# Kernel optimization log

Hardware: AMD Instinct MI355X
Metric: run time of the kernel (lower is better)

Reference implementation:

```python
import jax, jax.numpy as jnp
import numpy as np

DIM = 256
HEADS = 8
HEAD_DIM = DIM // HEADS
WS = 7            # window size
SHIFT = 3         # shift size
H = 56
W = 56
B = 32
WA = WS * WS      # window area = 49
NWH, NWW = H // WS, W // WS
NW = NWH * NWW    # windows per image


def _make_attn_mask():
    # replicate the torch mask construction for the shifted windows
    img = np.zeros((H, W), dtype=np.float32)
    cnt = 0
    for hs in (slice(0, -WS), slice(-WS, -SHIFT), slice(-SHIFT, None)):
        for ws_ in (slice(0, -WS), slice(-WS, -SHIFT), slice(-SHIFT, None)):
            img[hs, ws_] = cnt
            cnt += 1
    mw = img.reshape(NWH, WS, NWW, WS).transpose(0, 2, 1, 3).reshape(-1, WA)  # (nW, 49)
    diff = mw[:, None, :] - mw[:, :, None]                                    # (nW, 49, 49)
    return np.where(diff != 0, -100.0, 0.0).astype(np.float32)


def _make_rel_index():
    coords = np.stack(np.meshgrid(np.arange(WS), np.arange(WS), indexing='ij')).reshape(2, -1)
    rel = coords[:, :, None] - coords[:, None, :]        # (2, 49, 49)
    rel = rel.transpose(1, 2, 0) + (WS - 1)              # shift to >= 0
    rel[..., 0] *= 2 * WS - 1
    return rel.sum(-1).astype(np.int32)                  # (49, 49) in [0, 169)


def setup_inputs() -> dict:
    key = jax.random.key(0)
    ks = jax.random.split(key, 12)
    s = 0.02
    inp = {
        'x': jax.random.normal(ks[0], (B, H, W, DIM), dtype=jnp.float32),
        'ln1_w': jnp.ones((DIM,), jnp.float32), 'ln1_b': jnp.zeros((DIM,), jnp.float32),
        'qkv_w': s * jax.random.normal(ks[1], (3 * DIM, DIM), jnp.float32),
        'qkv_b': jnp.zeros((3 * DIM,), jnp.float32),
        'rpb_table': s * jax.random.normal(ks[2], ((2 * WS - 1) ** 2, HEADS), jnp.float32),
        'proj_w': s * jax.random.normal(ks[3], (DIM, DIM), jnp.float32),
        'proj_b': jnp.zeros((DIM,), jnp.float32),
        'ln2_w': jnp.ones((DIM,), jnp.float32), 'ln2_b': jnp.zeros((DIM,), jnp.float32),
        'fc1_w': s * jax.random.normal(ks[4], (4 * DIM, DIM), jnp.float32),
        'fc1_b': jnp.zeros((4 * DIM,), jnp.float32),
        'ln3_w': jnp.ones((4 * DIM,), jnp.float32), 'ln3_b': jnp.zeros((4 * DIM,), jnp.float32),
        'fc2_w': s * jax.random.normal(ks[5], (DIM, 4 * DIM), jnp.float32),
        'fc2_b': jnp.zeros((DIM,), jnp.float32),
        'attn_mask': jnp.asarray(_make_attn_mask()),     # (nW, 49, 49)
        'rel_index': jnp.asarray(_make_rel_index()),     # (49, 49) int32
    }
    return inp


def _ln(x, w, b, eps=1e-5):
    m = jnp.mean(x, axis=-1, keepdims=True)
    v = jnp.mean((x - m) ** 2, axis=-1, keepdims=True)
    return (x - m) * jax.lax.rsqrt(v + eps) * w + b


def reference(x, ln1_w, ln1_b, qkv_w, qkv_b, rpb_table, proj_w, proj_b,
              ln2_w, ln2_b, fc1_w, fc1_b, ln3_w, ln3_b, fc2_w, fc2_b,
              attn_mask, rel_index):
    Bn, Hn, Wn, C = x.shape
    # ---- attention branch ----
    y = _ln(x, ln1_w, ln1_b)
    sh = jnp.roll(y, (-SHIFT, -SHIFT), axis=(1, 2))
    # window partition: (B, H, W, C) -> (B*nW, 49, C)
    win = sh.reshape(Bn, NWH, WS, NWW, WS, C).transpose(0, 1, 3, 2, 4, 5).reshape(Bn * NW, WA, C)
    qkv = win @ qkv_w.T + qkv_b                              # (Bw, 49, 3C)
    qkv = qkv.reshape(Bn * NW, WA, 3, HEADS, HEAD_DIM).transpose(2, 0, 3, 1, 4)
    q, k, v = qkv[0], qkv[1], qkv[2]                         # (Bw, h, 49, d)
    scale = HEAD_DIM ** -0.5
    attn = jnp.einsum('bhqd,bhkd->bhqk', q * scale, k)       # (Bw, h, 49, 49)
    bias = rpb_table[rel_index]                              # (49, 49, h)
    attn = attn + jnp.transpose(bias, (2, 0, 1))[None]
    attn = attn.reshape(Bn, NW, HEADS, WA, WA) + attn_mask[None, :, None]
    attn = jax.nn.softmax(attn, axis=-1).reshape(Bn * NW, HEADS, WA, WA)
    out = jnp.einsum('bhqk,bhkd->bhqd', attn, v)             # (Bw, h, 49, d)
    out = out.transpose(0, 2, 1, 3).reshape(Bn * NW, WA, C)
    out = out @ proj_w.T + proj_b
    # window reverse + un-shift
    out = out.reshape(Bn, NWH, NWW, WS, WS, C).transpose(0, 1, 3, 2, 4, 5).reshape(Bn, Hn, Wn, C)
    out = jnp.roll(out, (SHIFT, SHIFT), axis=(1, 2))
    x = x + out
    # ---- MLP branch (note: extra LayerNorm inside MLP per source) ----
    z = _ln(x, ln2_w, ln2_b)
    h = jax.nn.gelu(z @ fc1_w.T + fc1_b, approximate=False)
    h = _ln(h, ln3_w, ln3_b)
    x = x + (h @ fc2_w.T + fc2_b)
    return x
```

## Files before the change

kernel.cpp:

```cpp
#include <hip/hip_runtime.h>
#include <hip/hip_bf16.h>
#include <math.h>

typedef __attribute__((ext_vector_type(8))) short bf16x8;
typedef __attribute__((ext_vector_type(4))) float f32x4;
typedef __attribute__((ext_vector_type(4))) float f4;
typedef __attribute__((ext_vector_type(8))) unsigned short us8;
typedef __attribute__((ext_vector_type(4))) unsigned short us4;
typedef unsigned short u16;
typedef unsigned int u32;

#define HEADS 8
#define SHIFT_ 3
#define HIMG 56
#define WIMG 56
#define WA 49
#define NTOK 100352
#define NPAIR 16384

static __device__ __forceinline__ float bf2f(u16 v){ return __uint_as_float(((u32)v)<<16); }
static __device__ __forceinline__ u16 f2bf(float f){
  u32 u = __float_as_uint(f);
  return (u16)((u + 0x7fffu + ((u>>16)&1u)) >> 16);
}
static __device__ __forceinline__ float wsum(float v){
  #pragma unroll
  for (int off=32; off>0; off>>=1) v += __shfl_xor(v, off, 64);
  return v;
}
static __device__ __forceinline__ void glds16(const u16* g, u16* l){
  __builtin_amdgcn_global_load_lds(
      (const __attribute__((address_space(1))) unsigned int*)g,
      (__attribute__((address_space(3))) unsigned int*)l, 16, 0, 0);
}
static __device__ __forceinline__ int tok2pix(int row){
  int bw = row / 49, t = row - bw*49;
  int b  = bw >> 6,  w = bw & 63;
  int wh = w >> 3,   ww = w & 7;
  int th = t / 7,    tw = t - th*7;
  int r = wh*7 + th + SHIFT_; if (r >= HIMG) r -= HIMG;
  int c = ww*7 + tw + SHIFT_; if (c >= WIMG) c -= WIMG;
  return (b*HIMG + r)*WIMG + c;
}
static __device__ __forceinline__ float gelu_f(float x){
  float x2 = x*x;
  float u  = x*(0.7978845608028654f + 0.0356774081363001f*x2);
  float e  = __expf(u+u);
  float th = 1.0f - 2.0f*__builtin_amdgcn_rcpf(1.0f+e);
  return 0.5f*x*(1.0f+th);
}

template<int C, int ISBF>
__global__ void ln_stats_kernel(const void* __restrict__ srcv, float* __restrict__ stats){
  int wave = threadIdx.x >> 6, lane = threadIdx.x & 63;
  int tok = blockIdx.x*4 + wave;
  float s=0.f, s2=0.f;
  if (ISBF == 0){
    const float* p = (const float*)srcv + (size_t)tok*C;
    #pragma unroll
    for (int i=0;i<C/256;i++){
      f4 v = *(const f4*)(p + lane*4*(C/256) + i*4);
      #pragma unroll
      for (int e=0;e<4;e++){ float f=v[e]; s+=f; s2+=f*f; }
    }
  } else {
    const u16* p = (const u16*)srcv + (size_t)tok*C;
    #pragma unroll
    for (int i=0;i<C/512;i++){
      us8 v = *(const us8*)(p + lane*8*(C/512) + i*8);
      #pragma unroll
      for (int e=0;e<8;e++){ float f=bf2f(v[e]); s+=f; s2+=f*f; }
    }
  }
  s = wsum(s); s2 = wsum(s2);
  if (lane==0){
    float mean = s/(float)C;
    float var  = s2/(float)C - mean*mean;
    stats[2*tok]   = mean;
    stats[2*tok+1] = rsqrtf(var + 1e-5f);
  }
}

__global__ void ln_apply_kernel(const float* __restrict__ src, u16* __restrict__ dst){
  int wave = threadIdx.x >> 6, lane = threadIdx.x & 63;
  int tok = blockIdx.x*4 + wave;
  const float* p = src + (size_t)tok*256;
  f4 a = *(const f4*)(p + lane*4);
  float s = a[0]+a[1]+a[2]+a[3];
  float s2 = a[0]*a[0]+a[1]*a[1]+a[2]*a[2]+a[3]*a[3];
  s = wsum(s); s2 = wsum(s2);
  float mean = s*(1.f/256.f);
  float var  = s2*(1.f/256.f) - mean*mean;
  float rstd = rsqrtf(var + 1e-5f);
  us4 o;
  #pragma unroll
  for (int e=0;e<4;e++) o[e] = f2bf((a[e]-mean)*rstd);
  *(us4*)(dst + (size_t)tok*256 + lane*4) = o;
}

__global__ void prep_weights(
    const float* __restrict__ qkv_w, const float* __restrict__ qkv_b,
    const float* __restrict__ ln1w,  const float* __restrict__ ln1b,
    const float* __restrict__ fc1_w, const float* __restrict__ fc1_b,
    const float* __restrict__ ln2w,  const float* __restrict__ ln2b,
    const float* __restrict__ fc2_w, const float* __restrict__ fc2_b,
    const float* __restrict__ ln3w,  const float* __restrict__ ln3b,
    const float* __restrict__ proj_w, const float* __restrict__ proj_b,
    u16* __restrict__ wq, float* __restrict__ bq,
    u16* __restrict__ w1, float* __restrict__ b1,
    u16* __restrict__ w2, float* __restrict__ b2,
    u16* __restrict__ wp, float* __restrict__ bp,
    float* __restrict__ cs2)
{
  int wave = threadIdx.x>>6, lane = threadIdx.x&63;
  int n = blockIdx.x*4 + wave;
  const float *W,*lw,*lb,*bs; u16* WO; float* BO; int K, row, noln, docs;
  if (n < 768)      { W=qkv_w; lw=ln1w; lb=ln1b; bs=qkv_b; WO=wq; BO=bq; K=256;  row=n;      noln=0; docs=0; }
  else if (n < 1792){ W=fc1_w; lw=ln2w; lb=ln2b; bs=fc1_b; WO=w1; BO=b1; K=256;  row=n-768;  noln=0; docs=0; }
  else if (n < 2048){ W=fc2_w; lw=ln3w; lb=ln3b; bs=fc2_b; WO=w2; BO=b2; K=1024; row=n-1792; noln=0; docs=1; }
  else              { W=proj_w; lw=nullptr; lb=nullptr; bs=proj_b; WO=wp; BO=bp; K=256; row=n-2048; noln=1; docs=0; }
  float dot = 0.f, cs = 0.f;
  for (int k=lane; k<K; k+=64){
    float wv = W[(size_t)row*K + k];
    if (noln){
      WO[(size_t)row*K + k] = f2bf(wv);
    } else {
      dot += wv * lb[k];
      u16 q = f2bf(wv * lw[k]);
      WO[(size_t)row*K + k] = q;
      cs += bf2f(q);
    }
  }
  dot = wsum(dot);
  if (docs){ cs = wsum(cs); if (lane==0) cs2[row] = cs; }
  if (lane==0) BO[row] = bs[row] + dot;
}

template<int SMODE, int EPI>
__global__ __launch_bounds__(256)
void gemm6(const void* __restrict__ Av, const u16* __restrict__ Bt,
           const float* __restrict__ stats, const float* __restrict__ biasf,
           const float* __restrict__ resid, const float* __restrict__ colsum,
           void* __restrict__ outv, int K, int NT, int CHUNK)
{
  constexpr int BM=128, BN=128, BK=64;
  __shared__ u16 smem[16384];
  u16* As = smem;
  u16* Bs = smem + 8192;
  int b = blockIdx.x;
  int linear = (b & 7)*CHUNK + (b >> 3);
  int mt = linear / NT, nt = linear - mt*NT;
  int m0 = mt*BM, n0 = nt*BN;
  int tid  = threadIdx.x;
  int lane = tid & 63, wave = tid >> 6;
  int wr = wave >> 1, wc = wave & 1;
  int lc16 = lane & 15, g = lane >> 4;
  int nsteps = K >> 6;

  const u16* asrc[4];
  const u16* bsrc[4];
  #pragma unroll
  for (int i=0;i<4;i++){
    int c = tid + i*256;
    int row = c >> 3, ch = (c & 7) ^ (row & 7);
    if (SMODE <= 1){
      int grow = (SMODE==0) ? tok2pix(m0+row) : (m0+row);
      asrc[i] = (const u16*)Av + (size_t)grow*K + ch*8;
    }
    bsrc[i] = Bt + (size_t)(n0+row)*K + ch*8;
  }
  float smean[4], srstd[4];
  if (SMODE == 3){
    #pragma unroll
    for (int i=0;i<4;i++){
      int grow = m0 + ((tid + i*256) >> 3);
      smean[i] = stats[2*grow]; srstd[i] = stats[2*grow+1];
    }
  }

  f32x4 acc[4][4];
  #pragma unroll
  for (int i=0;i<4;i++)
    #pragma unroll
    for (int j=0;j<4;j++){ acc[i][j][0]=0.f; acc[i][j][1]=0.f; acc[i][j][2]=0.f; acc[i][j][3]=0.f; }

  f4 rcurf[4][2];
  if (SMODE == 3){
    #pragma unroll
    for (int i=0;i<4;i++){
      int c = tid + i*256; int row = c>>3, ch = c&7;
      const float* ap = (const float*)Av + (size_t)(m0+row)*K + ch*8;
      rcurf[i][0] = *(const f4*)ap; rcurf[i][1] = *(const f4*)(ap+4);
    }
  }

  for (int t=0; t<nsteps; ++t){
    int kt = t << 6;
    if (SMODE <= 1){
      #pragma unroll
      for (int i=0;i<4;i++) glds16(asrc[i]+kt, As + i*2048 + wave*512);
    } else {
      #pragma unroll
      for (int i=0;i<4;i++){
        int c = tid + i*256; int row = c>>3, ch = c&7;
        us8 o;
        #pragma unroll
        for (int e=0;e<8;e++){
          float fv = rcurf[i][e>>2][e&3];
          o[e] = f2bf((fv - smean[i])*srstd[i]);
        }
        u32 byte = (u32)(row*128 + ch*16) ^ ((u32)(row&7)<<4);
        *(us8*)(As + (byte>>1)) = o;
      }
    }
    #pragma unroll
    for (int i=0;i<4;i++) glds16(bsrc[i]+kt, Bs + i*2048 + wave*512);
    __syncthreads();
    if (SMODE == 3 && t+1 < nsteps){
      int kt1 = kt + 64;
      f4 rnextf[4][2];
      #pragma unroll
      for (int i=0;i<4;i++){
        int c = tid + i*256; int row = c>>3, ch = c&7;
        const float* ap = (const float*)Av + (size_t)(m0+row)*K + kt1 + ch*8;
        rnextf[i][0] = *(const f4*)ap; rnextf[i][1] = *(const f4*)(ap+4);
      }
      #pragma unroll
      for (int kk=0; kk<2; kk++){
        bf16x8 af[4], bfr[4];
        #pragma unroll
        for (int mi=0;mi<4;mi++){
          int r = wr*64 + mi*16 + lc16;
          u32 byte = (u32)(r*128 + kk*64 + g*16) ^ ((u32)(r&7)<<4);
          af[mi] = *(const bf16x8*)(As + (byte>>1));
        }
        #pragma unroll
        for (int ni=0;ni<4;ni++){
          int r = wc*64 + ni*16 + lc16;
          u32 byte = (u32)(r*128 + kk*64 + g*16) ^ ((u32)(r&7)<<4);
          bfr[ni] = *(const bf16x8*)(Bs + (byte>>1));
        }
        #pragma unroll
        for (int mi=0;mi<4;mi++)
          #pragma unroll
          for (int ni=0;ni<4;ni++)
            acc[mi][ni] = __builtin_amdgcn_mfma_f32_16x16x32_bf16(af[mi], bfr[ni], acc[mi][ni], 0, 0, 0);
      }
      #pragma unroll
      for (int i=0;i<4;i++){ rcurf[i][0] = rnextf[i][0]; rcurf[i][1] = rnextf[i][1]; }
    } else {
      #pragma unroll
      for (int kk=0; kk<2; kk++){
        bf16x8 af[4], bfr[4];
        #pragma unroll
        for (int mi=0;mi<4;mi++){
          int r = wr*64 + mi*16 + lc16;
          u32 byte = (u32)(r*128 + kk*64 + g*16) ^ ((u32)(r&7)<<4);
          af[mi] = *(const bf16x8*)(As + (byte>>1));
        }
        #pragma unroll
        for (int ni=0;ni<4;ni++){
          int r = wc*64 + ni*16 + lc16;
          u32 byte = (u32)(r*128 + kk*64 + g*16) ^ ((u32)(r&7)<<4);
          bfr[ni] = *(const bf16x8*)(Bs + (byte>>1));
        }
        #pragma unroll
        for (int mi=0;mi<4;mi++)
          #pragma unroll
          for (int ni=0;ni<4;ni++)
            acc[mi][ni] = __builtin_amdgcn_mfma_f32_16x16x32_bf16(af[mi], bfr[ni], acc[mi][ni], 0, 0, 0);
      }
    }
    __syncthreads();
  }

  int lr = lane >> 4;
  if (EPI==0 || EPI==2){
    u16* Cs = smem;
    #pragma unroll
    for (int mi=0;mi<4;mi++){
      #pragma unroll
      for (int ni=0;ni<4;ni++){
        int cl = wc*64 + ni*16 + lc16;
        float bv = biasf[n0 + cl];
        #pragma unroll
        for (int j=0;j<4;j++){
          int rl = wr*64 + mi*16 + lr*4 + j;
          float v = acc[mi][ni][j] + bv;
          if (EPI==2) v = gelu_f(v);
          u32 byte = (u32)(rl*256 + cl*2) ^ ((u32)(rl&7)<<4);
          Cs[byte>>1] = f2bf(v);
        }
      }
    }
    __syncthreads();
    #pragma unroll
    for (int i=0;i<8;i++){
      int c = tid + i*256;
      int rl = c>>4, c0 = (c&15)*8;
      u32 byte = (u32)(rl*256 + c0*2) ^ ((u32)(rl&7)<<4);
      us8 v = *(const us8*)(Cs + (byte>>1));
      int row = m0 + rl, col = n0 + c0;
      if (EPI==0){
        int which = col>>8, hh = (col>>5)&7, d0 = col&31;
        int bwi = row/49, t = row - bwi*49;
        *(us8*)((u16*)outv + ((size_t)which*NPAIR + bwi*8 + hh)*(WA*32) + t*32 + d0) = v;
      } else {
        *(us8*)((u16*)outv + (size_t)row*1024 + col) = v;
      }
    }
  } else {
    float* Cs = (float*)smem;
    #pragma unroll
    for (int hp=0; hp<2; hp++){
      if (hp) __syncthreads();
      if (wc == hp){
        float bv4[4], cs4[4];
        #pragma unroll
        for (int ni=0;ni<4;ni++){
          int col = n0 + hp*64 + ni*16 + lc16;
          bv4[ni] = biasf[col];
          if (EPI==4) cs4[ni] = colsum[col];
        }
        #pragma unroll
        for (int mi=0;mi<4;mi++){
          #pragma unroll
          for (int j=0;j<4;j++){
            int rl = wr*64 + mi*16 + lr*4 + j;
            float rs = 1.f, mmrs = 0.f;
            if (EPI==4){
              int grow = m0 + rl;
              rs = stats[2*grow+1];
              mmrs = stats[2*grow]*rs;
            }
            #pragma unroll
            for (int ni=0;ni<4;ni++){
              int cl = ni*16 + lc16;
              float v;
              if (EPI==4) v = acc[mi][ni][j]*rs + bv4[ni] - mmrs*cs4[ni];
              else        v = acc[mi][ni][j] + bv4[ni];
              u32 byte = (u32)(rl*256 + cl*4) ^ ((u32)(rl&7)<<4);
              *(float*)((char*)Cs + byte) = v;
            }
          }
        }
      }
      __syncthreads();
      #pragma unroll
      for (int i=0;i<8;i++){
        int c = tid + i*256;
        int row = c>>4, ch = c&15;
        u32 byte = (u32)(row*256 + ch*16) ^ ((u32)(row&7)<<4);
        f4 v = *(const f4*)((const char*)Cs + byte);
        int grow = m0 + row, col = n0 + hp*64 + ch*4;
        size_t addr;
        if (EPI==1) addr = (size_t)tok2pix(grow)*256 + col;
        else        addr = (size_t)grow*256 + col;
        f4 rr = *(const f4*)(resid + addr);
        v += rr;
        *(f4*)((float*)outv + addr) = v;
      }
    }
  }
}

__global__ void attn_mfma_kernel(
    const u16* __restrict__ qkv,
    const float* __restrict__ rpb,
    const int* __restrict__ rel,
    const float* __restrict__ mask,
    u16* __restrict__ outb)
{
  __shared__ u16 Kls[4][64*32];
  __shared__ u16 Vt [4][32*64];
  __shared__ u16 Pls[4][64*64];
  int wave = threadIdx.x>>6, lane = threadIdx.x&63;
  int pair = blockIdx.x*4 + wave;
  int bw = pair>>3, h = pair&7, w = bw&63;
  int lc = lane&15, g = lane>>4;
  const u16* qg = qkv + (size_t)pair*(WA*32);
  const u16* kg = qg + (size_t)NPAIR*(WA*32);
  const u16* vg = qg + (size_t)2*NPAIR*(WA*32);
  u16* Kp = &Kls[wave][0];
  u16* Vp = &Vt[wave][0];
  u16* Pp = &Pls[wave][0];

  #pragma unroll
  for (int i=0;i<4;i++){
    int idx = i*64 + lane;
    int r = idx>>2, seg = idx&3;
    us8 kv, vv;
    if (r < WA){
      kv = *(const us8*)(kg + r*32 + seg*8);
      vv = *(const us8*)(vg + r*32 + seg*8);
    } else {
      #pragma unroll
      for (int e=0;e<8;e++){ kv[e]=0; vv[e]=0; }
    }
    *(us8*)(Kp + r*32 + seg*8) = kv;
    #pragma unroll
    for (int e=0;e<8;e++){
      int d = seg*8 + e;
      u32 byte = ((u32)(d*128 + r*2)) ^ ((u32)(d&7)<<4);
      Vp[byte>>1] = vv[e];
    }
  }

  bf16x8 qa[4];
  #pragma unroll
  for (int mi=0;mi<4;mi++){
    int r = mi*16 + lc;
    if (r < WA) qa[mi] = *(const bf16x8*)(qg + r*32 + g*8);
    else { bf16x8 z;
           #pragma unroll
           for (int e=0;e<8;e++) z[e]=0; qa[mi]=z; }
  }

  f32x4 acc[4][4];
  #pragma unroll
  for (int i=0;i<4;i++)
    #pragma unroll
    for (int j=0;j<4;j++){ acc[i][j][0]=0.f; acc[i][j][1]=0.f; acc[i][j][2]=0.f; acc[i][j][3]=0.f; }
  __syncthreads();
  #pragma unroll
  for (int ni=0;ni<4;ni++){
    bf16x8 kb = *(const bf16x8*)(Kp + (ni*16+lc)*32 + g*8);
    #pragma unroll
    for (int mi=0;mi<4;mi++)
      acc[mi][ni] = __builtin_amdgcn_mfma_f32_16x16x32_bf16(qa[mi], kb, acc[mi][ni], 0, 0, 0);
  }

  const float scale = 0.17677669529663689f;
  float rinv[4][4];
  #pragma unroll
  for (int mi=0;mi<4;mi++){
    #pragma unroll
    for (int jr=0;jr<4;jr++){
      int i = mi*16 + g*4 + jr;
      float sv[4];
      #pragma unroll
      for (int ni=0;ni<4;ni++){
        int j = ni*16 + lc;
        float s;
        if (i < WA && j < WA){
          s = acc[mi][ni][jr]*scale + rpb[rel[i*WA+j]*8 + h] + mask[((size_t)w*WA + i)*WA + j];
        } else s = -1e9f;
        sv[ni] = s;
      }
      float mx = fmaxf(fmaxf(sv[0],sv[1]), fmaxf(sv[2],sv[3]));
      #pragma unroll
      for (int off=1; off<16; off<<=1) mx = fmaxf(mx, __shfl_xor(mx, off, 64));
      float sum = 0.f;
      #pragma unroll
      for (int ni=0;ni<4;ni++){ sv[ni] = __expf(sv[ni]-mx); sum += sv[ni]; }
      #pragma unroll
      for (int off=1; off<16; off<<=1) sum += __shfl_xor(sum, off, 64);
      rinv[mi][jr] = __builtin_amdgcn_rcpf(sum);
      #pragma unroll
      for (int ni=0;ni<4;ni++){
        int j = ni*16 + lc;
        u32 byte = ((u32)(i*128 + j*2)) ^ ((u32)(i&7)<<4);
        Pp[byte>>1] = f2bf(sv[ni]);
      }
    }
  }

  bf16x8 vb[2][2];
  #pragma unroll
  for (int kk=0;kk<2;kk++)
    #pragma unroll
    for (int ni=0;ni<2;ni++){
      int d = ni*16 + lc;
      u32 byte = ((u32)(d*128 + kk*64 + g*16)) ^ ((u32)(d&7)<<4);
      vb[kk][ni] = *(const bf16x8*)(Vp + (byte>>1));
    }
  f32x4 aco[4][2];
  #pragma unroll
  for (int i=0;i<4;i++)
    #pragma unroll
    for (int j=0;j<2;j++){ aco[i][j][0]=0.f; aco[i][j][1]=0.f; aco[i][j][2]=0.f; aco[i][j][3]=0.f; }
  #pragma unroll
  for (int mi=0;mi<4;mi++){
    int r = mi*16 + lc;
    #pragma unroll
    for (int kk=0;kk<2;kk++){
      u32 byte = ((u32)(r*128 + kk*64 + g*16)) ^ ((u32)(r&7)<<4);
      bf16x8 pa = *(const bf16x8*)(Pp + (byte>>1));
      #pragma unroll
      for (int ni=0;ni<2;ni++)
        aco[mi][ni] = __builtin_amdgcn_mfma_f32_16x16x32_bf16(pa, vb[kk][ni], aco[mi][ni], 0, 0, 0);
    }
  }

  u16* Op = Kp;
  #pragma unroll
  for (int mi=0;mi<4;mi++){
    #pragma unroll
    for (int jr=0;jr<4;jr++){
      int i = mi*16 + g*4 + jr;
      if (i < WA){
        float rv = rinv[mi][jr];
        #pragma unroll
        for (int ni=0;ni<2;ni++)
          Op[i*32 + ni*16 + lc] = f2bf(aco[mi][ni][jr]*rv);
      }
    }
  }
  __syncthreads();
  size_t obase = (size_t)(bw*WA)*256 + h*32;
  #pragma unroll
  for (int i=0;i<4;i++){
    int c = i*64 + lane;
    if (c < WA*4){
      int t = c>>2, seg = c&3;
      *(us8*)(outb + obase + (size_t)t*256 + seg*8) = *(const us8*)(Op + t*32 + seg*8);
    }
  }
}

extern "C" void kernel_launch(void* const* d_in, const int* in_sizes, int n_in,
                              void* d_out, int out_size, void* d_ws, size_t ws_size,
                              hipStream_t stream) {
  const float* x      = (const float*)d_in[0];
  const float* ln1w   = (const float*)d_in[1];
  const float* ln1b   = (const float*)d_in[2];
  const float* qkv_w  = (const float*)d_in[3];
  const float* qkv_b  = (const float*)d_in[4];
  const float* rpb    = (const float*)d_in[5];
  const float* proj_w = (const float*)d_in[6];
  const float* proj_b = (const float*)d_in[7];
  const float* ln2w   = (const float*)d_in[8];
  const float* ln2b   = (const float*)d_in[9];
  const float* fc1_w  = (const float*)d_in[10];
  const float* fc1_b  = (const float*)d_in[11];
  const float* ln3w   = (const float*)d_in[12];
  const float* ln3b   = (const float*)d_in[13];
  const float* fc2_w  = (const float*)d_in[14];
  const float* fc2_b  = (const float*)d_in[15];
  const float* amask  = (const float*)d_in[16];
  const int*   rel    = (const int*)d_in[17];
  float* out = (float*)d_out;

  char* ws = (char*)d_ws;
  float* statsC = (float*)(ws);
  float* statsB = (float*)(ws +  802816);
  float* bq     = (float*)(ws + 1605632);
  float* b1     = (float*)(ws + 1608704);
  float* b2     = (float*)(ws + 1612800);
  float* bp     = (float*)(ws + 1613824);
  float* cs2    = (float*)(ws + 1614848);
  u16*   wq     = (u16*)  (ws + 1615872);
  u16*   w1     = (u16*)  (ws + 2009088);
  u16*   w2     = (u16*)  (ws + 2533376);
  u16*   wp     = (u16*)  (ws + 3057664);
  const size_t P0 = 3188736;
  u16*   qkvbuf = (u16*)(ws + P0);
  u16*   attno  = (u16*)(ws + P0 + 154140672);
  u16*   xb     = (u16*)(ws + P0 + 154140672);
  u16*   hbuf   = (u16*)(ws + P0);
  u16*   x1b    = (u16*)(ws + P0 + 205520896);
  const int bigws = (ws_size >= (size_t)(P0 + 205520896ull + 51380224ull));

  prep_weights<<<576,256,0,stream>>>(qkv_w,qkv_b,ln1w,ln1b, fc1_w,fc1_b,ln2w,ln2b,
                                     fc2_w,fc2_b,ln3w,ln3b, proj_w,proj_b,
                                     wq,bq, w1,b1, w2,b2, wp,bp, cs2);
  ln_apply_kernel<<<NTOK/4,256,0,stream>>>(x, xb);
  gemm6<0,0><<<784*6,256,0,stream>>>(xb, wq, nullptr, bq, nullptr, nullptr, qkvbuf, 256, 6, 588);
  attn_mfma_kernel<<<NPAIR/4,256,0,stream>>>(qkvbuf, rpb, rel, amask, attno);
  gemm6<1,1><<<784*2,256,0,stream>>>(attno, wp, nullptr, bp, x, nullptr, out, 256, 2, 196);
  if (bigws){
    ln_apply_kernel<<<NTOK/4,256,0,stream>>>(out, x1b);
    gemm6<1,2><<<784*8,256,0,stream>>>(x1b, w1, nullptr, b1, nullptr, nullptr, hbuf, 256, 8, 784);
  } else {
    ln_stats_kernel<256,0><<<NTOK/4,256,0,stream>>>(out, statsB);
    gemm6<3,2><<<784*8,256,0,stream>>>(out, w1, statsB, b1, nullptr, nullptr, hbuf, 256, 8, 784);
  }
  ln_stats_kernel<1024,1><<<NTOK/4,256,0,stream>>>(hbuf, statsC);
  gemm6<1,4><<<784*2,256,0,stream>>>(hbuf, w2, statsC, b2, out, cs2, out, 1024, 2, 196);
}
```

Measured before the change: 626.7 us.

## Fuse fc1, GELU, LN3 stats and fc2 into one MLP kernel

Replaces the separate fc1 GEMM, the bf16 hidden buffer write, the LN3 stats pass and the fc2 GEMM with a single kernel. Each block owns 64 rows, computes the 1024-wide hidden in 128-column chunks held in shared memory, accumulates per-row sum and sum of squares, and feeds each chunk straight into fc2. LN3 is then applied in the epilogue using precomputed column sums. This removes the ~200MB hidden-tensor round trip and two launches. The cost is a small 64-row M tile with weights re-streamed from L2 for every block, large shared memory use, and lower occupancy.

```diff
diff --git a/kernel.cpp b/kernel.cpp
--- a/kernel.cpp
+++ b/kernel.cpp
@@ -48,37 +48,6 @@
   float e  = __expf(u+u);
   float th = 1.0f - 2.0f*__builtin_amdgcn_rcpf(1.0f+e);
   return 0.5f*x*(1.0f+th);
-}
-
-template<int C, int ISBF>
-__global__ void ln_stats_kernel(const void* __restrict__ srcv, float* __restrict__ stats){
-  int wave = threadIdx.x >> 6, lane = threadIdx.x & 63;
-  int tok = blockIdx.x*4 + wave;
-  float s=0.f, s2=0.f;
-  if (ISBF == 0){
-    const float* p = (const float*)srcv + (size_t)tok*C;
-    #pragma unroll
-    for (int i=0;i<C/256;i++){
-      f4 v = *(const f4*)(p + lane*4*(C/256) + i*4);
-      #pragma unroll
-      for (int e=0;e<4;e++){ float f=v[e]; s+=f; s2+=f*f; }
-    }
-  } else {
-    const u16* p = (const u16*)srcv + (size_t)tok*C;
-    #pragma unroll
-    for (int i=0;i<C/512;i++){
-      us8 v = *(const us8*)(p + lane*8*(C/512) + i*8);
-      #pragma unroll
-      for (int e=0;e<8;e++){ float f=bf2f(v[e]); s+=f; s2+=f*f; }
-    }
-  }
-  s = wsum(s); s2 = wsum(s2);
-  if (lane==0){
-    float mean = s/(float)C;
-    float var  = s2/(float)C - mean*mean;
-    stats[2*tok]   = mean;
-    stats[2*tok+1] = rsqrtf(var + 1e-5f);
-  }
 }
 
 __global__ void ln_apply_kernel(const float* __restrict__ src, u16* __restrict__ dst){
@@ -139,8 +108,7 @@
 template<int SMODE, int EPI>
 __global__ __launch_bounds__(256)
 void gemm6(const void* __restrict__ Av, const u16* __restrict__ Bt,
-           const float* __restrict__ stats, const float* __restrict__ biasf,
-           const float* __restrict__ resid, const float* __restrict__ colsum,
+           const float* __restrict__ biasf, const float* __restrict__ resid,
            void* __restrict__ outv, int K, int NT, int CHUNK)
 {
   constexpr int BM=128, BN=128, BK=64;
@@ -163,119 +131,50 @@
   for (int i=0;i<4;i++){
     int c = tid + i*256;
     int row = c >> 3, ch = (c & 7) ^ (row & 7);
-    if (SMODE <= 1){
-      int grow = (SMODE==0) ? tok2pix(m0+row) : (m0+row);
-      asrc[i] = (const u16*)Av + (size_t)grow*K + ch*8;
-    }
+    int grow = (SMODE==0) ? tok2pix(m0+row) : (m0+row);
+    asrc[i] = (const u16*)Av + (size_t)grow*K + ch*8;
     bsrc[i] = Bt + (size_t)(n0+row)*K + ch*8;
   }
-  float smean[4], srstd[4];
-  if (SMODE == 3){
-    #pragma unroll
-    for (int i=0;i<4;i++){
-      int grow = m0 + ((tid + i*256) >> 3);
-      smean[i] = stats[2*grow]; srstd[i] = stats[2*grow+1];
-    }
-  }
 
   f32x4 acc[4][4];
   #pragma unroll
   for (int i=0;i<4;i++)
     #pragma unroll
     for (int j=0;j<4;j++){ acc[i][j][0]=0.f; acc[i][j][1]=0.f; acc[i][j][2]=0.f; acc[i][j][3]=0.f; }
-
-  f4 rcurf[4][2];
-  if (SMODE == 3){
-    #pragma unroll
-    for (int i=0;i<4;i++){
-      int c = tid + i*256; int row = c>>3, ch = c&7;
-      const float* ap = (const float*)Av + (size_t)(m0+row)*K + ch*8;
-      rcurf[i][0] = *(const f4*)ap; rcurf[i][1] = *(const f4*)(ap+4);
-    }
-  }
 
   for (int t=0; t<nsteps; ++t){
     int kt = t << 6;
-    if (SMODE <= 1){
-      #pragma unroll
-      for (int i=0;i<4;i++) glds16(asrc[i]+kt, As + i*2048 + wave*512);
-    } else {
-      #pragma unroll
-      for (int i=0;i<4;i++){
-        int c = tid + i*256; int row = c>>3, ch = c&7;
-        us8 o;
-        #pragma unroll
-        for (int e=0;e<8;e++){
-          float fv = rcurf[i][e>>2][e&3];
-          o[e] = f2bf((fv - smean[i])*srstd[i]);
-        }
-        u32 byte = (u32)(row*128 + ch*16) ^ ((u32)(row&7)<<4);
-        *(us8*)(As + (byte>>1)) = o;
-      }
-    }
+    #pragma unroll
+    for (int i=0;i<4;i++) glds16(asrc[i]+kt, As + i*2048 + wave*512);
     #pragma unroll
     for (int i=0;i<4;i++) glds16(bsrc[i]+kt, Bs + i*2048 + wave*512);
     __syncthreads();
-    if (SMODE == 3 && t+1 < nsteps){
-      int kt1 = kt + 64;
-      f4 rnextf[4][2];
-      #pragma unroll
-      for (int i=0;i<4;i++){
-        int c = tid + i*256; int row = c>>3, ch = c&7;
-        const float* ap = (const float*)Av + (size_t)(m0+row)*K + kt1 + ch*8;
-        rnextf[i][0] = *(const f4*)ap; rnextf[i][1] = *(const f4*)(ap+4);
-      }
-      #pragma unroll
-      for (int kk=0; kk<2; kk++){
-        bf16x8 af[4], bfr[4];
-        #pragma unroll
-        for (int mi=0;mi<4;mi++){
-          int r = wr*64 + mi*16 + lc16;
-          u32 byte = (u32)(r*128 + kk*64 + g*16) ^ ((u32)(r&7)<<4);
-          af[mi] = *(const bf16x8*)(As + (byte>>1));
-        }
-        #pragma unroll
-        for (int ni=0;ni<4;ni++){
-          int r = wc*64 + ni*16 + lc16;
-          u32 byte = (u32)(r*128 + kk*64 + g*16) ^ ((u32)(r&7)<<4);
-          bfr[ni] = *(const bf16x8*)(Bs + (byte>>1));
-        }
-        #pragma unroll
-        for (int mi=0;mi<4;mi++)
-          #pragma unroll
-          for (int ni=0;ni<4;ni++)
-            acc[mi][ni] = __builtin_amdgcn_mfma_f32_16x16x32_bf16(af[mi], bfr[ni], acc[mi][ni], 0, 0, 0);
-      }
-      #pragma unroll
-      for (int i=0;i<4;i++){ rcurf[i][0] = rnextf[i][0]; rcurf[i][1] = rnextf[i][1]; }
-    } else {
-      #pragma unroll
-      for (int kk=0; kk<2; kk++){
-        bf16x8 af[4], bfr[4];
-        #pragma unroll
-        for (int mi=0;mi<4;mi++){
-          int r = wr*64 + mi*16 + lc16;
-          u32 byte = (u32)(r*128 + kk*64 + g*16) ^ ((u32)(r&7)<<4);
-          af[mi] = *(const bf16x8*)(As + (byte>>1));
-        }
-        #pragma unroll
-        for (int ni=0;ni<4;ni++){
-          int r = wc*64 + ni*16 + lc16;
-          u32 byte = (u32)(r*128 + kk*64 + g*16) ^ ((u32)(r&7)<<4);
-          bfr[ni] = *(const bf16x8*)(Bs + (byte>>1));
-        }
-        #pragma unroll
-        for (int mi=0;mi<4;mi++)
-          #pragma unroll
-          for (int ni=0;ni<4;ni++)
-            acc[mi][ni] = __builtin_amdgcn_mfma_f32_16x16x32_bf16(af[mi], bfr[ni], acc[mi][ni], 0, 0, 0);
-      }
+    #pragma unroll
+    for (int kk=0; kk<2; kk++){
+      bf16x8 af[4], bfr[4];
+      #pragma unroll
+      for (int mi=0;mi<4;mi++){
+        int r = wr*64 + mi*16 + lc16;
+        u32 byte = (u32)(r*128 + kk*64 + g*16) ^ ((u32)(r&7)<<4);
+        af[mi] = *(const bf16x8*)(As + (byte>>1));
+      }
+      #pragma unroll
+      for (int ni=0;ni<4;ni++){
+        int r = wc*64 + ni*16 + lc16;
+        u32 byte = (u32)(r*128 + kk*64 + g*16) ^ ((u32)(r&7)<<4);
+        bfr[ni] = *(const bf16x8*)(Bs + (byte>>1));
+      }
+      #pragma unroll
+      for (int mi=0;mi<4;mi++)
+        #pragma unroll
+        for (int ni=0;ni<4;ni++)
+          acc[mi][ni] = __builtin_amdgcn_mfma_f32_16x16x32_bf16(af[mi], bfr[ni], acc[mi][ni], 0, 0, 0);
     }
     __syncthreads();
   }
 
   int lr = lane >> 4;
-  if (EPI==0 || EPI==2){
+  if (EPI==0){
     u16* Cs = smem;
     #pragma unroll
     for (int mi=0;mi<4;mi++){
@@ -287,7 +186,6 @@
         for (int j=0;j<4;j++){
           int rl = wr*64 + mi*16 + lr*4 + j;
           float v = acc[mi][ni][j] + bv;
-          if (EPI==2) v = gelu_f(v);
           u32 byte = (u32)(rl*256 + cl*2) ^ ((u32)(rl&7)<<4);
           Cs[byte>>1] = f2bf(v);
         }
@@ -301,13 +199,9 @@
       u32 byte = (u32)(rl*256 + c0*2) ^ ((u32)(rl&7)<<4);
       us8 v = *(const us8*)(Cs + (byte>>1));
       int row = m0 + rl, col = n0 + c0;
-      if (EPI==0){
-        int which = col>>8, hh = (col>>5)&7, d0 = col&31;
-        int bwi = row/49, t = row - bwi*49;
-        *(us8*)((u16*)outv + ((size_t)which*NPAIR + bwi*8 + hh)*(WA*32) + t*32 + d0) = v;
-      } else {
-        *(us8*)((u16*)outv + (size_t)row*1024 + col) = v;
-      }
+      int which = col>>8, hh = (col>>5)&7, d0 = col&31;
+      int bwi = row/49, t = row - bwi*49;
+      *(us8*)((u16*)outv + ((size_t)which*NPAIR + bwi*8 + hh)*(WA*32) + t*32 + d0) = v;
     }
   } else {
     float* Cs = (float*)smem;
@@ -315,32 +209,17 @@
     for (int hp=0; hp<2; hp++){
       if (hp) __syncthreads();
       if (wc == hp){
-        float bv4[4], cs4[4];
-        #pragma unroll
-        for (int ni=0;ni<4;ni++){
-          int col = n0 + hp*64 + ni*16 + lc16;
-          bv4[ni] = biasf[col];
-          if (EPI==4) cs4[ni] = colsum[col];
-        }
         #pragma unroll
         for (int mi=0;mi<4;mi++){
           #pragma unroll
-          for (int j=0;j<4;j++){
-            int rl = wr*64 + mi*16 + lr*4 + j;
-            float rs = 1.f, mmrs = 0.f;
-            if (EPI==4){
-              int grow = m0 + rl;
-              rs = stats[2*grow+1];
-              mmrs = stats[2*grow]*rs;
-            }
+          for (int ni=0;ni<4;ni++){
+            int cl = ni*16 + lc16;
+            float bv = biasf[n0 + hp*64 + cl];
             #pragma unroll
-            for (int ni=0;ni<4;ni++){
-              int cl = ni*16 + lc16;
-              float v;
-              if (EPI==4) v = acc[mi][ni][j]*rs + bv4[ni] - mmrs*cs4[ni];
-              else        v = acc[mi][ni][j] + bv4[ni];
+            for (int j=0;j<4;j++){
+              int rl = wr*64 + mi*16 + lr*4 + j;
               u32 byte = (u32)(rl*256 + cl*4) ^ ((u32)(rl&7)<<4);
-              *(float*)((char*)Cs + byte) = v;
+              *(float*)((char*)Cs + byte) = acc[mi][ni][j] + bv;
             }
           }
         }
@@ -353,14 +232,213 @@
         u32 byte = (u32)(row*256 + ch*16) ^ ((u32)(row&7)<<4);
         f4 v = *(const f4*)((const char*)Cs + byte);
         int grow = m0 + row, col = n0 + hp*64 + ch*4;
-        size_t addr;
-        if (EPI==1) addr = (size_t)tok2pix(grow)*256 + col;
-        else        addr = (size_t)grow*256 + col;
+        size_t addr = (size_t)tok2pix(grow)*256 + col;
         f4 rr = *(const f4*)(resid + addr);
         v += rr;
         *(f4*)((float*)outv + addr) = v;
       }
     }
+  }
+}
+
+__global__ __launch_bounds__(256)
+void mlp_fused(const u16* __restrict__ x1b, const u16* __restrict__ w1, const float* __restrict__ b1,
+               const u16* __restrict__ w2, const float* __restrict__ b2, const float* __restrict__ cs2,
+               float* __restrict__ out)
+{
+  __shared__ u16 smem[49664];
+  u16* Ax  = smem;
+  u16* W1s = smem + 16384;
+  u16* hcs = smem + 24576;
+  u16* W2s = smem + 32768;
+  float* statsP = (float*)(smem + 49152);
+
+  int b = blockIdx.x;
+  int linear = (b & 7)*196 + (b >> 3);
+  int m0 = linear * 64;
+  int tid = threadIdx.x, lane = tid & 63, wave = tid >> 6;
+  int wr = wave >> 1, wc = wave & 1;
+  int lc = lane & 15, g = lane >> 4;
+
+  #pragma unroll
+  for (int i=0;i<8;i++){
+    int c = tid + i*256;
+    int row = c >> 5, ch = (c & 31) ^ (row & 7);
+    glds16(x1b + (size_t)(m0+row)*256 + ch*8, Ax + i*2048 + wave*512);
+  }
+
+  f32x4 zacc[2][8];
+  #pragma unroll
+  for (int i=0;i<2;i++)
+    #pragma unroll
+    for (int j=0;j<8;j++){ zacc[i][j][0]=0.f; zacc[i][j][1]=0.f; zacc[i][j][2]=0.f; zacc[i][j][3]=0.f; }
+  float srow[2][4], s2row[2][4];
+  #pragma unroll
+  for (int i=0;i<2;i++)
+    #pragma unroll
+    for (int j=0;j<4;j++){ srow[i][j]=0.f; s2row[i][j]=0.f; }
+
+  for (int nt=0; nt<8; ++nt){
+    f32x4 hacc[2][4];
+    #pragma unroll
+    for (int i=0;i<2;i++)
+      #pragma unroll
+      for (int j=0;j<4;j++){ hacc[i][j][0]=0.f; hacc[i][j][1]=0.f; hacc[i][j][2]=0.f; hacc[i][j][3]=0.f; }
+    float b1r[4];
+    #pragma unroll
+    for (int nn=0;nn<4;nn++) b1r[nn] = b1[nt*128 + wc*64 + nn*16 + lc];
+
+    for (int t=0;t<4;++t){
+      #pragma unroll
+      for (int i=0;i<4;i++){
+        int c = tid + i*256;
+        int row = c >> 3, ch = (c & 7) ^ (row & 7);
+        glds16(w1 + (size_t)(nt*128+row)*256 + t*64 + ch*8, W1s + i*2048 + wave*512);
+      }
+      __syncthreads();
+      #pragma unroll
+      for (int kk=0;kk<2;kk++){
+        bf16x8 af[2], bfr[4];
+        #pragma unroll
+        for (int mi=0;mi<2;mi++){
+          int r = wr*32 + mi*16 + lc;
+          u32 byte = (u32)(r*512 + t*128 + kk*64 + g*16) ^ ((u32)(r&7)<<4);
+          af[mi] = *(const bf16x8*)(Ax + (byte>>1));
+        }
+        #pragma unroll
+        for (int nn=0;nn<4;nn++){
+          int r = wc*64 + nn*16 + lc;
+          u32 byte = (u32)(r*128 + kk*64 + g*16) ^ ((u32)(r&7)<<4);
+          bfr[nn] = *(const bf16x8*)(W1s + (byte>>1));
+        }
+        #pragma unroll
+        for (int mi=0;mi<2;mi++)
+          #pragma unroll
+          for (int nn=0;nn<4;nn++)
+            hacc[mi][nn] = __builtin_amdgcn_mfma_f32_16x16x32_bf16(af[mi], bfr[nn], hacc[mi][nn], 0, 0, 0);
+      }
+      __syncthreads();
+    }
+    #pragma unroll
+    for (int mi=0;mi<2;mi++){
+      #pragma unroll
+      for (int nn=0;nn<4;nn++){
+        #pragma unroll
+        for (int j=0;j<4;j++){
+          float v = gelu_f(hacc[mi][nn][j] + b1r[nn]);
+          srow[mi][j] += v; s2row[mi][j] += v*v;
+          int row = wr*32 + mi*16 + g*4 + j;
+          int col = wc*64 + nn*16 + lc;
+          u32 byte = (u32)(row*256 + col*2) ^ ((u32)(row&7)<<4);
+          hcs[byte>>1] = f2bf(v);
+        }
+      }
+    }
+    __syncthreads();
+    for (int ks=0;ks<2;++ks){
+      #pragma unroll
+      for (int i=0;i<8;i++){
+        int c = tid + i*256;
+        int row = c >> 3, ch = (c & 7) ^ (row & 7);
+        glds16(w2 + (size_t)row*1024 + nt*128 + ks*64 + ch*8, W2s + i*2048 + wave*512);
+      }
+      __syncthreads();
+      #pragma unroll
+      for (int kk=0;kk<2;kk++){
+        bf16x8 af[2], bfr[8];
+        #pragma unroll
+        for (int mi=0;mi<2;mi++){
+          int r = wr*32 + mi*16 + lc;
+          u32 byte = (u32)(r*256 + ks*128 + kk*64 + g*16) ^ ((u32)(r&7)<<4);
+          af[mi] = *(const bf16x8*)(hcs + (byte>>1));
+        }
+        #pragma unroll
+        for (int n=0;n<8;n++){
+          int r = wc*128 + n*16 + lc;
+          u32 byte = (u32)(r*128 + kk*64 + g*16) ^ ((u32)(r&7)<<4);
+          bfr[n] = *(const bf16x8*)(W2s + (byte>>1));
+        }
+        #pragma unroll
+        for (int mi=0;mi<2;mi++)
+          #pragma unroll
+          for (int n=0;n<8;n++)
+            zacc[mi][n] = __builtin_amdgcn_mfma_f32_16x16x32_bf16(af[mi], bfr[n], zacc[mi][n], 0, 0, 0);
+      }
+      __syncthreads();
+    }
+  }
+
+  #pragma unroll
+  for (int mi=0;mi<2;mi++){
+    #pragma unroll
+    for (int j=0;j<4;j++){
+      float s = srow[mi][j], q = s2row[mi][j];
+      #pragma unroll
+      for (int off=1; off<16; off<<=1){ s += __shfl_xor(s, off, 64); q += __shfl_xor(q, off, 64); }
+      srow[mi][j] = s; s2row[mi][j] = q;
+    }
+  }
+  if (wc==0 && lc==0){
+    #pragma unroll
+    for (int mi=0;mi<2;mi++)
+      #pragma unroll
+      for (int j=0;j<4;j++){
+        int row = wr*32 + mi*16 + g*4 + j;
+        statsP[row*2]   = srow[mi][j];
+        statsP[row*2+1] = s2row[mi][j];
+      }
+  }
+  __syncthreads();
+  if (wc==1 && lc==0){
+    #pragma unroll
+    for (int mi=0;mi<2;mi++)
+      #pragma unroll
+      for (int j=0;j<4;j++){
+        int row = wr*32 + mi*16 + g*4 + j;
+        float s = statsP[row*2]   + srow[mi][j];
+        float q = statsP[row*2+1] + s2row[mi][j];
+        float mean = s*(1.f/1024.f);
+        float var  = q*(1.f/1024.f) - mean*mean;
+        statsP[row*2]   = mean;
+        statsP[row*2+1] = rsqrtf(var + 1e-5f);
+      }
+  }
+  __syncthreads();
+
+  float* Cs = (float*)smem;
+  float csr[8], b2r[8];
+  #pragma unroll
+  for (int n=0;n<8;n++){
+    int col = wc*128 + n*16 + lc;
+    csr[n] = cs2[col]; b2r[n] = b2[col];
+  }
+  #pragma unroll
+  for (int mi=0;mi<2;mi++){
+    #pragma unroll
+    for (int j=0;j<4;j++){
+      int row = wr*32 + mi*16 + g*4 + j;
+      float mean = statsP[row*2], rstd = statsP[row*2+1];
+      float mr = mean*rstd;
+      #pragma unroll
+      for (int n=0;n<8;n++){
+        float v = zacc[mi][n][j]*rstd - mr*csr[n] + b2r[n];
+        int col = wc*128 + n*16 + lc;
+        u32 byte = (u32)(row*1024 + col*4) ^ ((u32)(row&7)<<4);
+        *(float*)((char*)Cs + byte) = v;
+      }
+    }
+  }
+  __syncthreads();
+  #pragma unroll
+  for (int i=0;i<16;i++){
+    int c = tid + i*256;
+    int row = c >> 6, ch = c & 63;
+    u32 byte = (u32)(row*1024 + ch*16) ^ ((u32)(row&7)<<4);
+    f4 v = *(const f4*)((const char*)Cs + byte);
+    size_t addr = (size_t)(m0+row)*256 + ch*4;
+    f4 rr = *(const f4*)(out + addr);
+    v += rr;
+    *(f4*)(out + addr) = v;
   }
 }
 
@@ -542,39 +620,28 @@
   float* out = (float*)d_out;
 
   char* ws = (char*)d_ws;
-  float* statsC = (float*)(ws);
-  float* statsB = (float*)(ws +  802816);
-  float* bq     = (float*)(ws + 1605632);
-  float* b1     = (float*)(ws + 1608704);
-  float* b2     = (float*)(ws + 1612800);
-  float* bp     = (float*)(ws + 1613824);
-  float* cs2    = (float*)(ws + 1614848);
-  u16*   wq     = (u16*)  (ws + 1615872);
-  u16*   w1     = (u16*)  (ws + 2009088);
-  u16*   w2     = (u16*)  (ws + 2533376);
-  u16*   wp     = (u16*)  (ws + 3057664);
-  const size_t P0 = 3188736;
+  float* bq     = (float*)(ws);
+  float* b1     = (float*)(ws + 3072);
+  float* b2     = (float*)(ws + 7168);
+  float* bp     = (float*)(ws + 8192);
+  float* cs2    = (float*)(ws + 9216);
+  u16*   wq     = (u16*)  (ws + 10240);
+  u16*   w1     = (u16*)  (ws + 403456);
+  u16*   w2     = (u16*)  (ws + 927744);
+  u16*   wp     = (u16*)  (ws + 1452032);
+  const size_t P0 = 1583104;
   u16*   qkvbuf = (u16*)(ws + P0);
   u16*   attno  = (u16*)(ws + P0 + 154140672);
   u16*   xb     = (u16*)(ws + P0 + 154140672);
-  u16*   hbuf   = (u16*)(ws + P0);
-  u16*   x1b    = (u16*)(ws + P0 + 205520896);
-  const int bigws = (ws_size >= (size_t)(P0 + 205520896ull + 51380224ull));
+  u16*   x1b    = (u16*)(ws + P0);
 
   prep_weights<<<576,256,0,stream>>>(qkv_w,qkv_b,ln1w,ln1b, fc1_w,fc1_b,ln2w,ln2b,
                                      fc2_w,fc2_b,ln3w,ln3b, proj_w,proj_b,
                                      wq,bq, w1,b1, w2,b2, wp,bp, cs2);
   ln_apply_kernel<<<NTOK/4,256,0,stream>>>(x, xb);
-  gemm6<0,0><<<784*6,256,0,stream>>>(xb, wq, nullptr, bq, nullptr, nullptr, qkvbuf, 256, 6, 588);
+  gemm6<0,0><<<784*6,256,0,stream>>>(xb, wq, bq, nullptr, qkvbuf, 256, 6, 588);
   attn_mfma_kernel<<<NPAIR/4,256,0,stream>>>(qkvbuf, rpb, rel, amask, attno);
-  gemm6<1,1><<<784*2,256,0,stream>>>(attno, wp, nullptr, bp, x, nullptr, out, 256, 2, 196);
-  if (bigws){
-    ln_apply_kernel<<<NTOK/4,256,0,stream>>>(out, x1b);
-    gemm6<1,2><<<784*8,256,0,stream>>>(x1b, w1, nullptr, b1, nullptr, nullptr, hbuf, 256, 8, 784);
-  } else {
-    ln_stats_kernel<256,0><<<NTOK/4,256,0,stream>>>(out, statsB);
-    gemm6<3,2><<<784*8,256,0,stream>>>(out, w1, statsB, b1, nullptr, nullptr, hbuf, 256, 8, 784);
-  }
-  ln_stats_kernel<1024,1><<<NTOK/4,256,0,stream>>>(hbuf, statsC);
-  gemm6<1,4><<<784*2,256,0,stream>>>(hbuf, w2, statsC, b2, out, cs2, out, 1024, 2, 196);
-}
+  gemm6<1,1><<<784*2,256,0,stream>>>(attno, wp, bp, x, out, 256, 2, 196);
+  ln_apply_kernel<<<NTOK/4,256,0,stream>>>(out, x1b);
+  mlp_fused<<<1568,256,0,stream>>>(x1b, w1, b1, w2, b2, cs2, out);
+}
```

Measured after the change: 699.9 us. +11.7%, slower.

## Fuse LN3 row statistics into fc1 GEMM epilogue via atomics

Applied to the files above, without the earlier changes.

Swaps the MFMA operand order so each lane holds four consecutive output columns of one row. That lets the epilogues do vectorized bias loads and LDS stores. The fc1+GELU epilogue now accumulates per-row sum and sum-of-squares of the GELU output and adds them atomically into a zeroed stats buffer. This removes the separate ln_stats pass over the 1024-wide bf16 hidden tensor, and the fc2 epilogue derives mean and rstd from those sums. The cost is an extra zeroing kernel, atomic contention across 8 column tiles per row, and the numerically weaker E[x²]-mean² variance computed from fp32 values rather than the stored bf16 ones.

```diff
diff --git a/kernel.cpp b/kernel.cpp
--- a/kernel.cpp
+++ b/kernel.cpp
@@ -48,6 +48,10 @@
   float e  = __expf(u+u);
   float th = 1.0f - 2.0f*__builtin_amdgcn_rcpf(1.0f+e);
   return 0.5f*x*(1.0f+th);
+}
+
+__global__ void zero_kernel(float* __restrict__ p){
+  p[blockIdx.x*256 + threadIdx.x] = 0.f;
 }
 
 template<int C, int ISBF>
@@ -138,10 +142,11 @@
 
 template<int SMODE, int EPI>
 __global__ __launch_bounds__(256)
-void gemm6(const void* __restrict__ Av, const u16* __restrict__ Bt,
-           const float* __restrict__ stats, const float* __restrict__ biasf,
-           const float* __restrict__ resid, const float* __restrict__ colsum,
-           void* __restrict__ outv, int K, int NT, int CHUNK)
+void gemm7(const void* __restrict__ Av, const u16* __restrict__ Bt,
+           const float* __restrict__ stats, float* __restrict__ hstats,
+           const float* __restrict__ biasf, const float* __restrict__ resid,
+           const float* __restrict__ colsum, void* __restrict__ outv,
+           int K, int NT, int CHUNK)
 {
   constexpr int BM=128, BN=128, BK=64;
   __shared__ u16 smem[16384];
@@ -244,7 +249,7 @@
         for (int mi=0;mi<4;mi++)
           #pragma unroll
           for (int ni=0;ni<4;ni++)
-            acc[mi][ni] = __builtin_amdgcn_mfma_f32_16x16x32_bf16(af[mi], bfr[ni], acc[mi][ni], 0, 0, 0);
+            acc[mi][ni] = __builtin_amdgcn_mfma_f32_16x16x32_bf16(bfr[ni], af[mi], acc[mi][ni], 0, 0, 0);
       }
       #pragma unroll
       for (int i=0;i<4;i++){ rcurf[i][0] = rnextf[i][0]; rcurf[i][1] = rnextf[i][1]; }
@@ -268,28 +273,39 @@
         for (int mi=0;mi<4;mi++)
           #pragma unroll
           for (int ni=0;ni<4;ni++)
-            acc[mi][ni] = __builtin_amdgcn_mfma_f32_16x16x32_bf16(af[mi], bfr[ni], acc[mi][ni], 0, 0, 0);
+            acc[mi][ni] = __builtin_amdgcn_mfma_f32_16x16x32_bf16(bfr[ni], af[mi], acc[mi][ni], 0, 0, 0);
       }
     }
     __syncthreads();
   }
 
-  int lr = lane >> 4;
   if (EPI==0 || EPI==2){
     u16* Cs = smem;
     #pragma unroll
     for (int mi=0;mi<4;mi++){
+      int rl = wr*64 + mi*16 + lc16;
+      float ss = 0.f, sq = 0.f;
       #pragma unroll
       for (int ni=0;ni<4;ni++){
-        int cl = wc*64 + ni*16 + lc16;
-        float bv = biasf[n0 + cl];
+        int cl = wc*64 + ni*16 + g*4;
+        f4 bv = *(const f4*)(biasf + n0 + cl);
+        us4 o;
         #pragma unroll
         for (int j=0;j<4;j++){
-          int rl = wr*64 + mi*16 + lr*4 + j;
-          float v = acc[mi][ni][j] + bv;
-          if (EPI==2) v = gelu_f(v);
-          u32 byte = (u32)(rl*256 + cl*2) ^ ((u32)(rl&7)<<4);
-          Cs[byte>>1] = f2bf(v);
+          float v = acc[mi][ni][j] + bv[j];
+          if (EPI==2){ v = gelu_f(v); ss += v; sq += v*v; }
+          o[j] = f2bf(v);
+        }
+        u32 byte = (u32)(rl*256 + cl*2) ^ ((u32)(rl&7)<<4);
+        *(us4*)(Cs + (byte>>1)) = o;
+      }
+      if (EPI==2){
+        ss += __shfl_xor(ss, 16, 64); ss += __shfl_xor(ss, 32, 64);
+        sq += __shfl_xor(sq, 16, 64); sq += __shfl_xor(sq, 32, 64);
+        if (g==0){
+          int grow = m0 + rl;
+          atomicAdd(&hstats[2*grow],   ss);
+          atomicAdd(&hstats[2*grow+1], sq);
         }
       }
     }
@@ -315,33 +331,34 @@
     for (int hp=0; hp<2; hp++){
       if (hp) __syncthreads();
       if (wc == hp){
-        float bv4[4], cs4[4];
-        #pragma unroll
-        for (int ni=0;ni<4;ni++){
-          int col = n0 + hp*64 + ni*16 + lc16;
-          bv4[ni] = biasf[col];
-          if (EPI==4) cs4[ni] = colsum[col];
-        }
         #pragma unroll
         for (int mi=0;mi<4;mi++){
+          int rl = wr*64 + mi*16 + lc16;
+          float rs = 1.f, mr = 0.f;
+          if (EPI==4){
+            int grow = m0 + rl;
+            float s = stats[2*grow], q = stats[2*grow+1];
+            float mean = s*(1.f/1024.f);
+            float var  = q*(1.f/1024.f) - mean*mean;
+            rs = rsqrtf(var + 1e-5f);
+            mr = mean*rs;
+          }
           #pragma unroll
-          for (int j=0;j<4;j++){
-            int rl = wr*64 + mi*16 + lr*4 + j;
-            float rs = 1.f, mmrs = 0.f;
+          for (int ni=0;ni<4;ni++){
+            int clb = ni*16 + g*4;
+            int col = n0 + hp*64 + clb;
+            f4 bv = *(const f4*)(biasf + col);
+            f4 v;
             if (EPI==4){
-              int grow = m0 + rl;
-              rs = stats[2*grow+1];
-              mmrs = stats[2*grow]*rs;
+              f4 cw = *(const f4*)(colsum + col);
+              #pragma unroll
+              for (int j=0;j<4;j++) v[j] = acc[mi][ni][j]*rs - mr*cw[j] + bv[j];
+            } else {
+              #pragma unroll
+              for (int j=0;j<4;j++) v[j] = acc[mi][ni][j] + bv[j];
             }
-            #pragma unroll
-            for (int ni=0;ni<4;ni++){
-              int cl = ni*16 + lc16;
-              float v;
-              if (EPI==4) v = acc[mi][ni][j]*rs + bv4[ni] - mmrs*cs4[ni];
-              else        v = acc[mi][ni][j] + bv4[ni];
-              u32 byte = (u32)(rl*256 + cl*4) ^ ((u32)(rl&7)<<4);
-              *(float*)((char*)Cs + byte) = v;
-            }
+            u32 byte = (u32)(rl*256 + clb*4) ^ ((u32)(rl&7)<<4);
+            *(f4*)((char*)Cs + byte) = v;
           }
         }
       }
@@ -542,7 +559,7 @@
   float* out = (float*)d_out;
 
   char* ws = (char*)d_ws;
-  float* statsC = (float*)(ws);
+  float* hstats = (float*)(ws);
   float* statsB = (float*)(ws +  802816);
   float* bq     = (float*)(ws + 1605632);
   float* b1     = (float*)(ws + 1608704);
@@ -565,16 +582,16 @@
                                      fc2_w,fc2_b,ln3w,ln3b, proj_w,proj_b,
                                      wq,bq, w1,b1, w2,b2, wp,bp, cs2);
   ln_apply_kernel<<<NTOK/4,256,0,stream>>>(x, xb);
-  gemm6<0,0><<<784*6,256,0,stream>>>(xb, wq, nullptr, bq, nullptr, nullptr, qkvbuf, 256, 6, 588);
+  gemm7<0,0><<<784*6,256,0,stream>>>(xb, wq, nullptr, nullptr, bq, nullptr, nullptr, qkvbuf, 256, 6, 588);
   attn_mfma_kernel<<<NPAIR/4,256,0,stream>>>(qkvbuf, rpb, rel, amask, attno);
-  gemm6<1,1><<<784*2,256,0,stream>>>(attno, wp, nullptr, bp, x, nullptr, out, 256, 2, 196);
+  gemm7<1,1><<<784*2,256,0,stream>>>(attno, wp, nullptr, nullptr, bp, x, nullptr, out, 256, 2, 196);
+  zero_kernel<<<784,256,0,stream>>>(hstats);
   if (bigws){
     ln_apply_kernel<<<NTOK/4,256,0,stream>>>(out, x1b);
-    gemm6<1,2><<<784*8,256,0,stream>>>(x1b, w1, nullptr, b1, nullptr, nullptr, hbuf, 256, 8, 784);
+    gemm7<1,2><<<784*8,256,0,stream>>>(x1b, w1, nullptr, hstats, b1, nullptr, nullptr, hbuf, 256, 8, 784);
   } else {
     ln_stats_kernel<256,0><<<NTOK/4,256,0,stream>>>(out, statsB);
-    gemm6<3,2><<<784*8,256,0,stream>>>(out, w1, statsB, b1, nullptr, nullptr, hbuf, 256, 8, 784);
-  }
-  ln_stats_kernel<1024,1><<<NTOK/4,256,0,stream>>>(hbuf, statsC);
-  gemm6<1,4><<<784*2,256,0,stream>>>(hbuf, w2, statsC, b2, out, cs2, out, 1024, 2, 196);
-}
+    gemm7<3,2><<<784*8,256,0,stream>>>(out, w1, statsB, hstats, b1, nullptr, nullptr, hbuf, 256, 8, 784);
+  }
+  gemm7<1,4><<<784*2,256,0,stream>>>(hbuf, w2, hstats, nullptr, b2, out, cs2, out, 1024, 2, 196);
+}
```

Result: slower. 659.0 us (+5.1%).
